# Kernel tuning notes

Hardware: AMD Instinct MI355X
Metric: run time of the kernel (lower is better)

## Reference

```python
import jax, jax.numpy as jnp
import numpy as np

SCALING_FACTOR = 1.0


def setup_inputs() -> dict:
    key = jax.random.key(0)
    k1, k2, k3 = jax.random.split(key, 3)
    B, N1, N2, DX, DZ, NT, NK = 4, 64, 64, 2, 128, 2048, 2
    x_grid = jax.random.uniform(k1, (B, N1, N2, DX), dtype=jnp.float32)
    z_grid = jax.random.normal(k2, (B, N1, N2, DZ), dtype=jnp.float32)
    xt = jax.random.uniform(k3, (B, NT, DX), dtype=jnp.float32)
    # Replicates torch init: logspace around log10(init_lengthscale), inverse-softplus
    init_ls = np.logspace(np.log10(0.1) - 0.5, np.log10(0.1) + 0.5, NK).astype(np.float32)
    init_ls = np.tile(init_ls[None, :], (DX, 1))  # (dim, num_kernels)
    lengthscale_param = jnp.asarray(np.log(np.expm1(init_ls)))
    return {"x_grid": x_grid, "z_grid": z_grid, "xt": xt, "lengthscale_param": lengthscale_param}


def reference(x_grid, z_grid, xt, lengthscale_param):
    B = x_grid.shape[0]
    xg = x_grid.reshape(B, -1, x_grid.shape[-1])   # (b, ng, dx)
    zg = z_grid.reshape(B, -1, z_grid.shape[-1])   # (b, ng, dz)
    ls = 1e-5 + jax.nn.softplus(lengthscale_param)  # (dx, nk)
    # EQ/RBF weights: (b, nt, ng, nk)
    diff = (xt[:, :, None, :, None] - xg[:, None, :, :, None]) / ls[None, None, None]
    weights = jnp.exp(-0.5 * jnp.sum(diff * diff, axis=3))
    # weighted smoothing: per-kernel matmul weights @ z_grid, then interleave as (dz nk)
    out = jnp.einsum('btgk,bgz->btzk', weights, zg) / SCALING_FACTOR  # (b, nt, dz, nk)
    return out.reshape(B, xt.shape[1], -1)  # (b, nt, dz*nk), nk fastest like 'b nt (dz nk)'
```

## Files before the change

kernel.cpp:

```cpp
#include <hip/hip_runtime.h>
#include <hip/hip_bf16.h>
#include <cmath>

#define B_   4
#define NT_  2048
#define G_   4096
#define DZ_  128

typedef __attribute__((ext_vector_type(8))) short bf16x8;
typedef __attribute__((ext_vector_type(4))) float f32x4;

__device__ __forceinline__ float softplus_f(float x) {
    return fmaxf(x, 0.0f) + log1pf(expf(-fabsf(x)));
}

__device__ __forceinline__ void gl2lds16(const void* gsrc, void* ldst) {
    __builtin_amdgcn_global_load_lds(
        (const __attribute__((address_space(1))) unsigned int*)gsrc,
        (__attribute__((address_space(3))) unsigned int*)ldst, 16, 0, 0);
}

__global__ __launch_bounds__(256, 1)
void transpose_z(const float* __restrict__ z, unsigned short* __restrict__ zt)
{
    __shared__ unsigned short tile[64][66];
    const int bx = blockIdx.x;
    const int zti = bx & 1;
    const int gt  = (bx >> 1) & 63;
    const int b   = bx >> 7;
    const int g0 = gt * 64, z0 = zti * 64;
    const int tid = threadIdx.x;
    const int zl = tid & 63, gl = tid >> 6;
    #pragma unroll
    for (int i = 0; i < 16; ++i) {
        const int g = gl + i * 4;
        const float v = z[(size_t)(b * G_ + g0 + g) * DZ_ + z0 + zl];
        unsigned int u = __float_as_uint(v);
        u = u + 0x7FFFu + ((u >> 16) & 1u);
        tile[g][zl] = (unsigned short)(u >> 16);
    }
    __syncthreads();
    const int gp = (tid & 31) * 2, zi = tid >> 5;
    const int c  = (g0 + gp) >> 5, gi = gp & 31;
    #pragma unroll
    for (int i = 0; i < 8; ++i) {
        const int zz = zi + i * 8;
        const unsigned int lo = tile[gp][zz], hi = tile[gp + 1][zz];
        *(unsigned int*)(zt + ((size_t)(b * 128 + c) * 128 + z0 + zz) * 32 + gi)
            = lo | (hi << 16);
    }
}

__global__ __launch_bounds__(256, 1)
void setconv_main(const float* __restrict__ xt,
                  const float* __restrict__ xg,
                  const float* __restrict__ lsp,
                  const unsigned short* __restrict__ Zt,
                  float* __restrict__ out)
{
    __shared__ __align__(16) unsigned short lds[32768];

    const int bx = blockIdx.x;
    const int b  = bx & 3;
    const int tt = bx >> 2;
    const int tid  = threadIdx.x;
    const int w    = tid >> 6;
    const int lane = tid & 63;
    const int quad = lane >> 4;
    const int l15  = lane & 15;
    const int t0   = tt * 32;

    float c00, c01, c10, c11;
    {
        const float h = -0.72134752f;
        float ls;
        ls = 1e-5f + softplus_f(lsp[0]); c00 = h / (ls * ls);
        ls = 1e-5f + softplus_f(lsp[1]); c01 = h / (ls * ls);
        ls = 1e-5f + softplus_f(lsp[2]); c10 = h / (ls * ls);
        ls = 1e-5f + softplus_f(lsp[3]); c11 = h / (ls * ls);
    }

    const float xtA0 = xt[(size_t)(b * NT_ + t0 + l15) * 2 + 0];
    const float xtA1 = xt[(size_t)(b * NT_ + t0 + l15) * 2 + 1];
    const float xtB0 = xt[(size_t)(b * NT_ + t0 + 16 + l15) * 2 + 0];
    const float xtB1 = xt[(size_t)(b * NT_ + t0 + 16 + l15) * 2 + 1];

    f32x4 acc[2][2][8];
    #pragma unroll
    for (int ts = 0; ts < 2; ++ts)
        #pragma unroll
        for (int k = 0; k < 2; ++k)
            #pragma unroll
            for (int n = 0; n < 8; ++n) acc[ts][k][n] = (f32x4)0.0f;

    unsigned short* const buf0 = lds + w * 8192;
    unsigned short* const buf1 = buf0 + 4096;
    const float* xgq = xg + (size_t)(b * G_ + w * 1024 + quad * 8) * 2;
    const unsigned short* zs = Zt + (size_t)(b * 128 + w * 32) * 4096 + lane * 8;

    float4 xv0 = *(const float4*)(xgq + 0);
    float4 xv1 = *(const float4*)(xgq + 4);
    float4 xv2 = *(const float4*)(xgq + 8);
    float4 xv3 = *(const float4*)(xgq + 12);
    #pragma unroll
    for (int i = 0; i < 8; ++i)
        gl2lds16(zs + i * 512, buf0 + i * 512);
    #pragma unroll
    for (int i = 0; i < 8; ++i)
        gl2lds16(zs + 4096 + i * 512, buf1 + i * 512);

    #define CHUNK_BODY(CH, TILE)                                               \
    {                                                                          \
        const int ch_ = (CH);                                                  \
        float gx[8], gy[8];                                                    \
        gx[0]=xv0.x; gy[0]=xv0.y; gx[1]=xv0.z; gy[1]=xv0.w;                    \
        gx[2]=xv1.x; gy[2]=xv1.y; gx[3]=xv1.z; gy[3]=xv1.w;                    \
        gx[4]=xv2.x; gy[4]=xv2.y; gx[5]=xv2.z; gy[5]=xv2.w;                    \
        gx[6]=xv3.x; gy[6]=xv3.y; gx[7]=xv3.z; gy[7]=xv3.w;                    \
        union { bf16x8 v; unsigned int u[4]; } aA0, aA1, aB0, aB1;             \
        {                                                                      \
            unsigned int w0b[8], w1b[8];                                       \
            _Pragma("unroll")                                                  \
            for (int j = 0; j < 8; ++j) {                                      \
                const float d0 = xtA0 - gx[j];                                 \
                const float d1 = xtA1 - gy[j];                                 \
                const float q0 = d0 * d0;                                      \
                const float q1 = d1 * d1;                                      \
                const float e0 = fmaf(q1, c10, q0 * c00);                      \
                const float e1 = fmaf(q1, c11, q0 * c01);                      \
                w0b[j] = __float_as_uint(__builtin_amdgcn_exp2f(e0));          \
                w1b[j] = __float_as_uint(__builtin_amdgcn_exp2f(e1));          \
            }                                                                  \
            _Pragma("unroll")                                                  \
            for (int h = 0; h < 4; ++h) {                                      \
                aA0.u[h] = __builtin_amdgcn_perm(w0b[2*h+1], w0b[2*h], 0x07060302u); \
                aA1.u[h] = __builtin_amdgcn_perm(w1b[2*h+1], w1b[2*h], 0x07060302u); \
            }                                                                  \
        }                                                                      \
        {                                                                      \
            unsigned int w0b[8], w1b[8];                                       \
            _Pragma("unroll")                                                  \
            for (int j = 0; j < 8; ++j) {                                      \
                const float d0 = xtB0 - gx[j];                                 \
                const float d1 = xtB1 - gy[j];                                 \
                const float q0 = d0 * d0;                                      \
                const float q1 = d1 * d1;                                      \
                const float e0 = fmaf(q1, c10, q0 * c00);                      \
                const float e1 = fmaf(q1, c11, q0 * c01);                      \
                w0b[j] = __float_as_uint(__builtin_amdgcn_exp2f(e0));          \
                w1b[j] = __float_as_uint(__builtin_amdgcn_exp2f(e1));          \
            }                                                                  \
            _Pragma("unroll")                                                  \
            for (int h = 0; h < 4; ++h) {                                      \
                aB0.u[h] = __builtin_amdgcn_perm(w0b[2*h+1], w0b[2*h], 0x07060302u); \
                aB1.u[h] = __builtin_amdgcn_perm(w1b[2*h+1], w1b[2*h], 0x07060302u); \
            }                                                                  \
        }                                                                      \
                       \
        __builtin_amdgcn_s_waitcnt(0x0F78);                      \
        if (ch_ < 31) {                                                        \
            const float* xp = xgq + (ch_ + 1) * 64;                            \
            xv0 = *(const float4*)(xp + 0);                                    \
            xv1 = *(const float4*)(xp + 4);                                    \
            xv2 = *(const float4*)(xp + 8);                                    \
            xv3 = *(const float4*)(xp + 12);                                   \
        }                                                                      \
        _Pragma("unroll")                                                      \
        for (int nt = 0; nt < 8; ++nt) {                                       \
            const bf16x8 bz = *(const bf16x8*)((TILE) + nt * 512 + l15 * 32 + quad * 8); \
            acc[0][0][nt] = __builtin_amdgcn_mfma_f32_16x16x32_bf16(aA0.v, bz, acc[0][0][nt], 0, 0, 0); \
            acc[0][1][nt] = __builtin_amdgcn_mfma_f32_16x16x32_bf16(aA1.v, bz, acc[0][1][nt], 0, 0, 0); \
            acc[1][0][nt] = __builtin_amdgcn_mfma_f32_16x16x32_bf16(aB0.v, bz, acc[1][0][nt], 0, 0, 0); \
            acc[1][1][nt] = __builtin_amdgcn_mfma_f32_16x16x32_bf16(aB1.v, bz, acc[1][1][nt], 0, 0, 0); \
        }                                                                      \
        if (ch_ < 30) {                                                        \
            const unsigned short* zc = zs + (size_t)(ch_ + 2) * 4096;          \
            _Pragma("unroll")                                                  \
            for (int i = 0; i < 8; ++i)                                        \
                gl2lds16(zc + i * 512, (TILE) + i * 512);                      \
        }                                                                      \
    }

    for (int p = 0; p < 16; ++p) {
        CHUNK_BODY(2 * p,     buf0);
        CHUNK_BODY(2 * p + 1, buf1);
    }
    #undef CHUNK_BODY

    float* const red = (float*)lds;
    #define RED_W(slot) { \
        float* bp = &red[(slot) * 8192 + lane * 4]; \
        _Pragma("unroll") \
        for (int ts = 0; ts < 2; ++ts) \
            _Pragma("unroll") \
            for (int k = 0; k < 2; ++k) \
                _Pragma("unroll") \
                for (int n = 0; n < 8; ++n) \
                    *(f32x4*)(bp + (ts * 16 + k * 8 + n) * 256) = acc[ts][k][n]; }
    #define RED_A(slot) { \
        const float* bp = &red[(slot) * 8192 + lane * 4]; \
        _Pragma("unroll") \
        for (int ts = 0; ts < 2; ++ts) \
            _Pragma("unroll") \
            for (int k = 0; k < 2; ++k) \
                _Pragma("unroll") \
                for (int n = 0; n < 8; ++n) \
                    acc[ts][k][n] += *(const f32x4*)(bp + (ts * 16 + k * 8 + n) * 256); }
    #define RED_W_T(slot, ts) { \
        float* bp = &red[(slot) * 8192 + lane * 4]; \
        _Pragma("unroll") \
        for (int k = 0; k < 2; ++k) \
            _Pragma("unroll") \
            for (int n = 0; n < 8; ++n) \
                *(f32x4*)(bp + (k * 8 + n) * 256) = acc[ts][k][n]; }
    #define RED_A_T(slot, ts) { \
        const float* bp = &red[(slot) * 8192 + lane * 4]; \
        _Pragma("unroll") \
        for (int k = 0; k < 2; ++k) \
            _Pragma("unroll") \
            for (int n = 0; n < 8; ++n) \
                acc[ts][k][n] += *(const f32x4*)(bp + (k * 8 + n) * 256); }

    __syncthreads();
    if (w >= 2) RED_W(w - 2);
    __syncthreads();
    if (w < 2) RED_A(w);
    if (w == 1) RED_W_T(0, 0);
    if (w == 0) RED_W_T(1, 1);
    __syncthreads();
    if (w < 2) {
        if (w == 0) { RED_A_T(0, 0); } else { RED_A_T(1, 1); }
        const int ts = w;
        const int tr = t0 + ts * 16 + quad * 4;
        #pragma unroll
        for (int nt = 0; nt < 8; ++nt) {
            float* ob = out + (size_t)(b * NT_ + tr) * (DZ_ * 2) + (nt * 16 + l15) * 2;
            #pragma unroll
            for (int r = 0; r < 4; ++r)
                *(float2*)(ob + (size_t)r * (DZ_ * 2)) =
                    make_float2(acc[ts][0][nt][r], acc[ts][1][nt][r]);
        }
    }
    #undef RED_W
    #undef RED_A
    #undef RED_W_T
    #undef RED_A_T
}

extern "C" void kernel_launch(void* const* d_in, const int* in_sizes, int n_in,
                              void* d_out, int out_size, void* d_ws, size_t ws_size,
                              hipStream_t stream)
{
    const float* x_grid = (const float*)d_in[0];
    const float* z_grid = (const float*)d_in[1];
    const float* xt     = (const float*)d_in[2];
    const float* lsp    = (const float*)d_in[3];
    float* out = (float*)d_out;
    unsigned short* Zt = (unsigned short*)d_ws;

    hipLaunchKernelGGL(transpose_z, dim3(512), dim3(256), 0, stream, z_grid, Zt);
    hipLaunchKernelGGL(setconv_main, dim3(256), dim3(256), 0, stream,
                       xt, x_grid, lsp, Zt, out);
}
```

Baseline: 121.5 us.

## Split target tiles across two wave groups with shared LDS staging

Blocks grow from 256 to 512 threads. Each wave now handles one 16-target sub-tile rather than two, and the pair of waves sharing a grid partition cooperatively stage the z chunk into shared LDS, half each. This halves the per-wave weight computation and accumulator registers and doubles the waves per CU, aiming to raise occupancy and hide latency. It adds block-wide barriers every chunk to coordinate the shared staging, and the reduction now takes more sync steps.

```diff
diff --git a/kernel.cpp b/kernel.cpp
--- a/kernel.cpp
+++ b/kernel.cpp
@@ -51,7 +51,7 @@
     }
 }
 
-__global__ __launch_bounds__(256, 1)
+__global__ __launch_bounds__(512, 2)
 void setconv_main(const float* __restrict__ xt,
                   const float* __restrict__ xg,
                   const float* __restrict__ lsp,
@@ -65,6 +65,8 @@
     const int tt = bx >> 2;
     const int tid  = threadIdx.x;
     const int w    = tid >> 6;
+    const int ts   = w >> 2;
+    const int p    = w & 3;
     const int lane = tid & 63;
     const int quad = lane >> 4;
     const int l15  = lane & 15;
@@ -80,34 +82,34 @@
         ls = 1e-5f + softplus_f(lsp[3]); c11 = h / (ls * ls);
     }
 
-    const float xtA0 = xt[(size_t)(b * NT_ + t0 + l15) * 2 + 0];
-    const float xtA1 = xt[(size_t)(b * NT_ + t0 + l15) * 2 + 1];
-    const float xtB0 = xt[(size_t)(b * NT_ + t0 + 16 + l15) * 2 + 0];
-    const float xtB1 = xt[(size_t)(b * NT_ + t0 + 16 + l15) * 2 + 1];
-
-    f32x4 acc[2][2][8];
+    const float xt0 = xt[(size_t)(b * NT_ + t0 + ts * 16 + l15) * 2 + 0];
+    const float xt1 = xt[(size_t)(b * NT_ + t0 + ts * 16 + l15) * 2 + 1];
+
+    f32x4 acc[2][8];
     #pragma unroll
-    for (int ts = 0; ts < 2; ++ts)
+    for (int k = 0; k < 2; ++k)
         #pragma unroll
-        for (int k = 0; k < 2; ++k)
-            #pragma unroll
-            for (int n = 0; n < 8; ++n) acc[ts][k][n] = (f32x4)0.0f;
-
-    unsigned short* const buf0 = lds + w * 8192;
-    unsigned short* const buf1 = buf0 + 4096;
-    const float* xgq = xg + (size_t)(b * G_ + w * 1024 + quad * 8) * 2;
-    const unsigned short* zs = Zt + (size_t)(b * 128 + w * 32) * 4096 + lane * 8;
+        for (int n = 0; n < 8; ++n) acc[k][n] = (f32x4)0.0f;
+
+    unsigned short* const slot0 = lds + p * 8192;
+    unsigned short* const slot1 = slot0 + 4096;
+    const float* xgq = xg + (size_t)(b * G_ + p * 1024 + quad * 8) * 2;
+    const unsigned short* zs = Zt + (size_t)(b * 128 + p * 32) * 4096
+                               + ts * 2048 + lane * 8;
+
+    #define STAGE(C, TILE) {                                                   \
+        const unsigned short* zc = zs + (size_t)(C) * 4096;                    \
+        _Pragma("unroll")                                                      \
+        for (int i = 0; i < 4; ++i)                                            \
+            gl2lds16(zc + i * 512, (TILE) + ts * 2048 + i * 512);              \
+    }
 
     float4 xv0 = *(const float4*)(xgq + 0);
     float4 xv1 = *(const float4*)(xgq + 4);
     float4 xv2 = *(const float4*)(xgq + 8);
     float4 xv3 = *(const float4*)(xgq + 12);
-    #pragma unroll
-    for (int i = 0; i < 8; ++i)
-        gl2lds16(zs + i * 512, buf0 + i * 512);
-    #pragma unroll
-    for (int i = 0; i < 8; ++i)
-        gl2lds16(zs + 4096 + i * 512, buf1 + i * 512);
+    STAGE(0, slot0);
+    STAGE(1, slot1);
 
     #define CHUNK_BODY(CH, TILE)                                               \
     {                                                                          \
@@ -117,13 +119,13 @@
         gx[2]=xv1.x; gy[2]=xv1.y; gx[3]=xv1.z; gy[3]=xv1.w;                    \
         gx[4]=xv2.x; gy[4]=xv2.y; gx[5]=xv2.z; gy[5]=xv2.w;                    \
         gx[6]=xv3.x; gy[6]=xv3.y; gx[7]=xv3.z; gy[7]=xv3.w;                    \
-        union { bf16x8 v; unsigned int u[4]; } aA0, aA1, aB0, aB1;             \
+        union { bf16x8 v; unsigned int u[4]; } a0, a1;                         \
         {                                                                      \
             unsigned int w0b[8], w1b[8];                                       \
             _Pragma("unroll")                                                  \
             for (int j = 0; j < 8; ++j) {                                      \
-                const float d0 = xtA0 - gx[j];                                 \
-                const float d1 = xtA1 - gy[j];                                 \
+                const float d0 = xt0 - gx[j];                                  \
+                const float d1 = xt1 - gy[j];                                  \
                 const float q0 = d0 * d0;                                      \
                 const float q1 = d1 * d1;                                      \
                 const float e0 = fmaf(q1, c10, q0 * c00);                      \
@@ -133,30 +135,11 @@
             }                                                                  \
             _Pragma("unroll")                                                  \
             for (int h = 0; h < 4; ++h) {                                      \
-                aA0.u[h] = __builtin_amdgcn_perm(w0b[2*h+1], w0b[2*h], 0x07060302u); \
-                aA1.u[h] = __builtin_amdgcn_perm(w1b[2*h+1], w1b[2*h], 0x07060302u); \
+                a0.u[h] = __builtin_amdgcn_perm(w0b[2*h+1], w0b[2*h], 0x07060302u); \
+                a1.u[h] = __builtin_amdgcn_perm(w1b[2*h+1], w1b[2*h], 0x07060302u); \
             }                                                                  \
         }                                                                      \
-        {                                                                      \
-            unsigned int w0b[8], w1b[8];                                       \
-            _Pragma("unroll")                                                  \
-            for (int j = 0; j < 8; ++j) {                                      \
-                const float d0 = xtB0 - gx[j];                                 \
-                const float d1 = xtB1 - gy[j];                                 \
-                const float q0 = d0 * d0;                                      \
-                const float q1 = d1 * d1;                                      \
-                const float e0 = fmaf(q1, c10, q0 * c00);                      \
-                const float e1 = fmaf(q1, c11, q0 * c01);                      \
-                w0b[j] = __float_as_uint(__builtin_amdgcn_exp2f(e0));          \
-                w1b[j] = __float_as_uint(__builtin_amdgcn_exp2f(e1));          \
-            }                                                                  \
-            _Pragma("unroll")                                                  \
-            for (int h = 0; h < 4; ++h) {                                      \
-                aB0.u[h] = __builtin_amdgcn_perm(w0b[2*h+1], w0b[2*h], 0x07060302u); \
-                aB1.u[h] = __builtin_amdgcn_perm(w1b[2*h+1], w1b[2*h], 0x07060302u); \
-            }                                                                  \
-        }                                                                      \
-                       \
+            \
         __builtin_amdgcn_s_waitcnt(0x0F78);                      \
         if (ch_ < 31) {                                                        \
             const float* xp = xgq + (ch_ + 1) * 64;                            \
@@ -165,72 +148,50 @@
             xv2 = *(const float4*)(xp + 8);                                    \
             xv3 = *(const float4*)(xp + 12);                                   \
         }                                                                      \
+        __builtin_amdgcn_s_barrier();       \
         _Pragma("unroll")                                                      \
         for (int nt = 0; nt < 8; ++nt) {                                       \
             const bf16x8 bz = *(const bf16x8*)((TILE) + nt * 512 + l15 * 32 + quad * 8); \
-            acc[0][0][nt] = __builtin_amdgcn_mfma_f32_16x16x32_bf16(aA0.v, bz, acc[0][0][nt], 0, 0, 0); \
-            acc[0][1][nt] = __builtin_amdgcn_mfma_f32_16x16x32_bf16(aA1.v, bz, acc[0][1][nt], 0, 0, 0); \
-            acc[1][0][nt] = __builtin_amdgcn_mfma_f32_16x16x32_bf16(aB0.v, bz, acc[1][0][nt], 0, 0, 0); \
-            acc[1][1][nt] = __builtin_amdgcn_mfma_f32_16x16x32_bf16(aB1.v, bz, acc[1][1][nt], 0, 0, 0); \
+            acc[0][nt] = __builtin_amdgcn_mfma_f32_16x16x32_bf16(a0.v, bz, acc[0][nt], 0, 0, 0); \
+            acc[1][nt] = __builtin_amdgcn_mfma_f32_16x16x32_bf16(a1.v, bz, acc[1][nt], 0, 0, 0); \
         }                                                                      \
-        if (ch_ < 30) {                                                        \
-            const unsigned short* zc = zs + (size_t)(ch_ + 2) * 4096;          \
-            _Pragma("unroll")                                                  \
-            for (int i = 0; i < 8; ++i)                                        \
-                gl2lds16(zc + i * 512, (TILE) + i * 512);                      \
-        }                                                                      \
-    }
-
-    for (int p = 0; p < 16; ++p) {
-        CHUNK_BODY(2 * p,     buf0);
-        CHUNK_BODY(2 * p + 1, buf1);
+        __builtin_amdgcn_s_waitcnt(0xC07F);                    \
+        __builtin_amdgcn_s_barrier();        \
+        if (ch_ < 30) STAGE(ch_ + 2, TILE);                                    \
+    }
+
+    for (int q = 0; q < 16; ++q) {
+        CHUNK_BODY(2 * q,     slot0);
+        CHUNK_BODY(2 * q + 1, slot1);
     }
     #undef CHUNK_BODY
+    #undef STAGE
 
     float* const red = (float*)lds;
     #define RED_W(slot) { \
-        float* bp = &red[(slot) * 8192 + lane * 4]; \
-        _Pragma("unroll") \
-        for (int ts = 0; ts < 2; ++ts) \
-            _Pragma("unroll") \
-            for (int k = 0; k < 2; ++k) \
-                _Pragma("unroll") \
-                for (int n = 0; n < 8; ++n) \
-                    *(f32x4*)(bp + (ts * 16 + k * 8 + n) * 256) = acc[ts][k][n]; }
-    #define RED_A(slot) { \
-        const float* bp = &red[(slot) * 8192 + lane * 4]; \
-        _Pragma("unroll") \
-        for (int ts = 0; ts < 2; ++ts) \
-            _Pragma("unroll") \
-            for (int k = 0; k < 2; ++k) \
-                _Pragma("unroll") \
-                for (int n = 0; n < 8; ++n) \
-                    acc[ts][k][n] += *(const f32x4*)(bp + (ts * 16 + k * 8 + n) * 256); }
-    #define RED_W_T(slot, ts) { \
-        float* bp = &red[(slot) * 8192 + lane * 4]; \
+        float* bp = &red[(slot) * 4096 + lane * 4]; \
         _Pragma("unroll") \
         for (int k = 0; k < 2; ++k) \
             _Pragma("unroll") \
             for (int n = 0; n < 8; ++n) \
-                *(f32x4*)(bp + (k * 8 + n) * 256) = acc[ts][k][n]; }
-    #define RED_A_T(slot, ts) { \
-        const float* bp = &red[(slot) * 8192 + lane * 4]; \
+                *(f32x4*)(bp + (k * 8 + n) * 256) = acc[k][n]; }
+    #define RED_A(slot) { \
+        const float* bp = &red[(slot) * 4096 + lane * 4]; \
         _Pragma("unroll") \
         for (int k = 0; k < 2; ++k) \
             _Pragma("unroll") \
             for (int n = 0; n < 8; ++n) \
-                acc[ts][k][n] += *(const f32x4*)(bp + (k * 8 + n) * 256); }
-
-    __syncthreads();
-    if (w >= 2) RED_W(w - 2);
-    __syncthreads();
-    if (w < 2) RED_A(w);
-    if (w == 1) RED_W_T(0, 0);
-    if (w == 0) RED_W_T(1, 1);
-    __syncthreads();
-    if (w < 2) {
-        if (w == 0) { RED_A_T(0, 0); } else { RED_A_T(1, 1); }
-        const int ts = w;
+                acc[k][n] += *(const f32x4*)(bp + (k * 8 + n) * 256); }
+
+    __syncthreads();
+    if (p >= 2) RED_W(ts * 2 + (p - 2));
+    __syncthreads();
+    if (p < 2) RED_A(ts * 2 + p);
+    __syncthreads();
+    if (p == 1) RED_W(ts);
+    __syncthreads();
+    if (p == 0) {
+        RED_A(ts);
         const int tr = t0 + ts * 16 + quad * 4;
         #pragma unroll
         for (int nt = 0; nt < 8; ++nt) {
@@ -238,13 +199,11 @@
             #pragma unroll
             for (int r = 0; r < 4; ++r)
                 *(float2*)(ob + (size_t)r * (DZ_ * 2)) =
-                    make_float2(acc[ts][0][nt][r], acc[ts][1][nt][r]);
+                    make_float2(acc[0][nt][r], acc[1][nt][r]);
         }
     }
     #undef RED_W
     #undef RED_A
-    #undef RED_W_T
-    #undef RED_A_T
 }
 
 extern "C" void kernel_launch(void* const* d_in, const int* in_sizes, int n_in,
@@ -259,6 +218,6 @@
     unsigned short* Zt = (unsigned short*)d_ws;
 
     hipLaunchKernelGGL(transpose_z, dim3(512), dim3(256), 0, stream, z_grid, Zt);
-    hipLaunchKernelGGL(setconv_main, dim3(256), dim3(256), 0, stream,
+    hipLaunchKernelGGL(setconv_main, dim3(256), dim3(512), 0, stream,
                        xt, x_grid, lsp, Zt, out);
 }
```

After: 114.5 us. 1.06x faster.
